# Kernel optimization log

Hardware: AMD Instinct MI355X
Metric: run time of the kernel (lower is better)

## Reference

```python
import jax, jax.numpy as jnp
import numpy as np

TOKEN_DIM = 768
HIDDEN_DIM = 384
PATCH_SCALE = 2
SELECTED_RATIO = 0.15


def setup_inputs() -> dict:
    key = jax.random.key(0)
    ks = jax.random.split(key, 12)
    B, T, D = 32, 1024, TOKEN_DIM
    Thr = T * PATCH_SCALE * PATCH_SCALE  # 4096
    flat_dim = D * PATCH_SCALE * PATCH_SCALE  # 3072
    H = HIDDEN_DIM
    s = lambda fan_in: 1.0 / np.sqrt(fan_in)
    inp = {
        "base_tokens": jax.random.normal(ks[0], (B, T, D), jnp.float32),
        "highres_tokens": jax.random.normal(ks[1], (B, Thr, D), jnp.float32),
        "selection_scores": jax.random.normal(ks[2], (B, T), jnp.float32),
        # local_refine: Linear(flat_dim,H) -> GELU -> Linear(H,D)
        "W1": jax.random.uniform(ks[3], (flat_dim, H), jnp.float32, -s(flat_dim), s(flat_dim)),
        "b1": jax.random.uniform(ks[4], (H,), jnp.float32, -s(flat_dim), s(flat_dim)),
        "W2": jax.random.uniform(ks[5], (H, D), jnp.float32, -s(H), s(H)),
        "b2": jax.random.uniform(ks[6], (D,), jnp.float32, -s(H), s(H)),
        # blend_gate: Linear(2D+1,H) -> SiLU -> Linear(H,1)
        "Wg1": jax.random.uniform(ks[7], (2 * D + 1, H), jnp.float32, -s(2 * D + 1), s(2 * D + 1)),
        "bg1": jax.random.uniform(ks[8], (H,), jnp.float32, -s(2 * D + 1), s(2 * D + 1)),
        "Wg2": jax.random.uniform(ks[9], (H, 1), jnp.float32, -s(H), s(H)),
        "bg2": jax.random.uniform(ks[10], (1,), jnp.float32, -s(H), s(H)),
    }
    return inp


def reference(base_tokens, highres_tokens, selection_scores,
              W1, b1, W2, b2, Wg1, bg1, Wg2, bg2):
    B, T, D = base_tokens.shape
    S = PATCH_SCALE
    g = int(round(np.sqrt(T)))  # coarse grid side
    # strided patch reshape: [B, g, S, g, S, D] -> [B, g, g, S, S, D] -> [B, T, S*S*D]
    local = highres_tokens.reshape(B, g, S, g, S, D)
    local = local.transpose(0, 1, 3, 2, 4, 5).reshape(B, T, S * S * D)
    # local refine MLP (exact-erf GELU matches torch nn.GELU default)
    h = jax.nn.gelu(jnp.einsum('btf,fh->bth', local, W1) + b1, approximate=False)
    refined_local = jnp.einsum('bth,hd->btd', h, W2) + b2
    # blend gate
    gate_in = jnp.concatenate([base_tokens, refined_local, selection_scores[..., None]], axis=-1)
    hg = jax.nn.silu(jnp.einsum('btf,fh->bth', gate_in, Wg1) + bg1)
    gate = jax.nn.sigmoid(jnp.einsum('bth,ho->bto', hg, Wg2) + bg2)  # [B, T, 1]
    # top-k selection mask (static k)
    topk = max(1, int(round(T * SELECTED_RATIO)))
    topk_idx = jax.lax.top_k(selection_scores, topk)[1]  # [B, k]
    mask = jnp.zeros((B, T), base_tokens.dtype).at[jnp.arange(B)[:, None], topk_idx].set(1.0)
    refined = base_tokens + mask[..., None] * gate * (refined_local - base_tokens)
    return refined
```

## Files before the change

kernel.cpp:

```cpp
#include <hip/hip_runtime.h>
#include <cstdint>

#define NB    32
#define NTOK  1024
#define D_    768
#define NHR   4096
#define HID   384
#define KSEL  154
#define MSEL  4928
#define MT_   77
#define FLAT  3072

typedef short  s16x8 __attribute__((ext_vector_type(8)));
typedef unsigned short u16x8 __attribute__((ext_vector_type(8)));
typedef unsigned short u16x4 __attribute__((ext_vector_type(4)));
typedef float  f32x4 __attribute__((ext_vector_type(4)));

__device__ inline unsigned short f2bf(float f) {
    uint32_t u = __builtin_bit_cast(uint32_t, f);
    u += 0x7FFFu + ((u >> 16) & 1u);
    return (unsigned short)(u >> 16);
}
__device__ inline float bf2f(unsigned short h) {
    uint32_t u = ((uint32_t)h) << 16;
    return __builtin_bit_cast(float, u);
}

#define OFF_SEL   0
#define OFF_W1T   32768
#define OFF_W2T   2392064
#define OFF_WG1T  2981888
#define OFF_ABASE 4161536
#define OFF_H     11730944
#define OFF_RL    15515648
#define OFF_HG    23085056
#define OFF_RMAP  30654464

__global__ __launch_bounds__(1024) void topk_kernel(const float* __restrict__ scores,
                                                    int* __restrict__ sel,
                                                    int* __restrict__ rmap) {
    __shared__ float s[NTOK];
    __shared__ int cnt;
    const int b = blockIdx.x;
    const int t = threadIdx.x;
    s[t] = scores[b * NTOK + t];
    if (t == 0) cnt = 0;
    __syncthreads();
    float v = s[t];
    int rank = 0;
    for (int j = 0; j < NTOK; ++j) {
        float vj = s[j];
        rank += (vj > v) || (vj == v && j < t);
    }
    int rm = -1;
    if (rank < KSEL) {
        int pos = atomicAdd(&cnt, 1);
        rm = b * KSEL + pos;
        sel[rm] = t;
    }
    rmap[b * NTOK + t] = rm;
}

__global__ __launch_bounds__(256) void tcvt_all(const float* __restrict__ W1,
                                                const float* __restrict__ W2,
                                                const float* __restrict__ Wg1,
                                                unsigned short* __restrict__ W1t,
                                                unsigned short* __restrict__ W2t,
                                                unsigned short* __restrict__ Wg1t) {
    __shared__ unsigned short T[64][66];
    int bid = blockIdx.x;
    const float* src; unsigned short* dst; int K, N, kt, nt;
    if (bid < 288)      { src = W1;  dst = W1t;  K = FLAT;   N = HID; nt = bid % 6;  kt = bid / 6;  }
    else if (bid < 360) { int l = bid - 288; src = W2;  dst = W2t;  K = HID;  N = D_;  nt = l % 12; kt = l / 12; }
    else                { int l = bid - 360; src = Wg1; dst = Wg1t; K = 1536; N = HID; nt = l % 6;  kt = l / 6;  }
    const int k0 = kt * 64, n0 = nt * 64;
    const int tid = threadIdx.x;
    {
        const int ln = tid & 63, kc = tid >> 6;
        #pragma unroll
        for (int j = 0; j < 16; ++j)
            T[ln][kc * 16 + j] = f2bf(src[(uint64_t)(k0 + kc * 16 + j) * N + n0 + ln]);
    }
    __syncthreads();
    {
        const int row = tid >> 2, c0 = (tid & 3) * 16;
        u16x8 v0, v1;
        #pragma unroll
        for (int p = 0; p < 8; ++p) { v0[p] = T[row][c0 + p]; v1[p] = T[row][c0 + 8 + p]; }
        *(u16x8*)(dst + (uint64_t)(n0 + row) * K + k0 + c0) = v0;
        *(u16x8*)(dst + (uint64_t)(n0 + row) * K + k0 + c0 + 8) = v1;
    }
}

__global__ __launch_bounds__(256) void gather_kernel(
    const int* __restrict__ sel, const float* __restrict__ highres,
    const float* __restrict__ base,
    unsigned short* __restrict__ Aloc, unsigned short* __restrict__ Abase) {
    const int r = blockIdx.x;
    const int b = r / KSEL;
    const int t = sel[r];
    const int gy = t >> 5, gx = t & 31;
    for (int ch = threadIdx.x; ch < 480; ch += 256) {
        if (ch < 384) {
            int k8 = ch * 8;
            int p = k8 / D_;
            int col = k8 - p * D_;
            int hr = (gy * 2 + (p >> 1)) * 64 + gx * 2 + (p & 1);
            const float4* s4 = (const float4*)(highres + ((uint64_t)b * NHR + hr) * D_ + col);
            float4 v0 = s4[0], v1 = s4[1];
            u16x8 v;
            v[0]=f2bf(v0.x); v[1]=f2bf(v0.y); v[2]=f2bf(v0.z); v[3]=f2bf(v0.w);
            v[4]=f2bf(v1.x); v[5]=f2bf(v1.y); v[6]=f2bf(v1.z); v[7]=f2bf(v1.w);
            *(u16x8*)(Aloc + (uint64_t)r * FLAT + k8) = v;
        } else {
            int col = (ch - 384) * 8;
            const float4* s4 = (const float4*)(base + ((uint64_t)b * NTOK + t) * D_ + col);
            float4 v0 = s4[0], v1 = s4[1];
            u16x8 v;
            v[0]=f2bf(v0.x); v[1]=f2bf(v0.y); v[2]=f2bf(v0.z); v[3]=f2bf(v0.w);
            v[4]=f2bf(v1.x); v[5]=f2bf(v1.y); v[6]=f2bf(v1.z); v[7]=f2bf(v1.w);
            *(u16x8*)(Abase + (uint64_t)r * D_ + col) = v;
        }
    }
}

template <int MODE>
__global__ __launch_bounds__(256) void gemm_mfma(
    const unsigned short* __restrict__ A0,
    const unsigned short* __restrict__ A1,
    const unsigned short* __restrict__ Bt,
    const float* __restrict__ bias,
    const int* __restrict__ sel,
    const float* __restrict__ scores,
    const float* __restrict__ WgLast,
    void* __restrict__ Cout)
{
    constexpr int K = MODE == 0 ? FLAT : (MODE == 1 ? HID : 2 * D_);
    constexpr int N = MODE == 1 ? D_ : HID;
    constexpr int NT = N / 64;
    constexpr int NSTEP = K / 64;

    const int lin = blockIdx.x;
    const int xcd = lin & 7;
    const int j   = lin >> 3;
    const int mhi = j / NT;
    const int ntile = j - mhi * NT;
    const int mt = mhi * 8 + xcd;
    if (mt >= MT_) return;
    const int m0 = mt * 64;
    const int n0 = ntile * 64;

    __shared__ unsigned short As[2][64 * 64];
    __shared__ unsigned short Bs[2][64 * 64];
    __shared__ float scv[64];

    const int tid = threadIdx.x;
    const int lane = tid & 63;
    const int wid = tid >> 6;
    const int wm = wid >> 1;
    const int wn = wid & 1;

    if (MODE == 2 && tid < 64) {
        int r = m0 + tid, b = r / KSEL, t = sel[r];
        scv[tid] = scores[b * NTOK + t];
    }

    const int sr0 = tid >> 3;
    const int sc0 = tid & 7;

    auto loadA = [&](int k0, int half, s16x8& dst) {
        int r = sr0 + half * 32;
        int k = k0 + sc0 * 8;
        const unsigned short* p;
        if (MODE == 2) {
            p = (k < D_) ? (A0 + (uint64_t)(m0 + r) * D_ + k)
                         : (A1 + (uint64_t)(m0 + r) * D_ + (k - D_));
        } else {
            p = A0 + (uint64_t)(m0 + r) * K + k;
        }
        dst = *(const s16x8*)p;
    };
    auto loadB = [&](int k0, int half, s16x8& dst) {
        int r = sr0 + half * 32;
        dst = *(const s16x8*)(Bt + (uint64_t)(n0 + r) * K + k0 + sc0 * 8);
    };
    auto writeTile = [&](int buf, s16x8* a, s16x8* b) {
        #pragma unroll
        for (int half = 0; half < 2; ++half) {
            int r = sr0 + half * 32;
            int c = sc0 ^ (r & 7);
            *(s16x8*)&As[buf][r * 64 + c * 8] = a[half];
            *(s16x8*)&Bs[buf][r * 64 + c * 8] = b[half];
        }
    };

    f32x4 acc[2][2];
    #pragma unroll
    for (int i = 0; i < 2; ++i)
        #pragma unroll
        for (int jj = 0; jj < 2; ++jj) acc[i][jj] = (f32x4){0.f, 0.f, 0.f, 0.f};

    s16x8 aR[2], bR[2];
    loadA(0, 0, aR[0]); loadA(0, 1, aR[1]);
    loadB(0, 0, bR[0]); loadB(0, 1, bR[1]);
    writeTile(0, aR, bR);
    __syncthreads();
    if (NSTEP > 1) {
        loadA(64, 0, aR[0]); loadA(64, 1, aR[1]);
        loadB(64, 0, bR[0]); loadB(64, 1, bR[1]);
    }

    int cur = 0;
    for (int t = 0; t < NSTEP; ++t) {
        #pragma unroll
        for (int kk = 0; kk < 2; ++kk) {
            s16x8 af[2], bfr[2];
            #pragma unroll
            for (int i = 0; i < 2; ++i) {
                int row  = wm * 32 + i * 16 + (lane & 15);
                int cch  = (kk * 4 + (lane >> 4)) ^ (row & 7);
                af[i] = *(const s16x8*)&As[cur][row * 64 + cch * 8];
                int nrow = wn * 32 + i * 16 + (lane & 15);
                int cchb = (kk * 4 + (lane >> 4)) ^ (nrow & 7);
                bfr[i] = *(const s16x8*)&Bs[cur][nrow * 64 + cchb * 8];
            }
            #pragma unroll
            for (int i = 0; i < 2; ++i)
                #pragma unroll
                for (int jj = 0; jj < 2; ++jj)
                    acc[i][jj] = __builtin_amdgcn_mfma_f32_16x16x32_bf16(af[i], bfr[jj], acc[i][jj], 0, 0, 0);
        }
        if (t + 1 < NSTEP) {
            writeTile(cur ^ 1, aR, bR);
            __syncthreads();
            if (t + 2 < NSTEP) {
                int k0 = (t + 2) * 64;
                loadA(k0, 0, aR[0]); loadA(k0, 1, aR[1]);
                loadB(k0, 0, bR[0]); loadB(k0, 1, bR[1]);
            }
            cur ^= 1;
        }
    }

    #pragma unroll
    for (int i = 0; i < 2; ++i) {
        #pragma unroll
        for (int jj = 0; jj < 2; ++jj) {
            #pragma unroll
            for (int reg = 0; reg < 4; ++reg) {
                int m = m0 + wm * 32 + i * 16 + (lane >> 4) * 4 + reg;
                int n = n0 + wn * 32 + jj * 16 + (lane & 15);
                float x = acc[i][jj][reg] + bias[n];
                if (MODE == 0) {
                    x = 0.5f * x * (1.0f + erff(x * 0.70710678118654752f));
                    ((unsigned short*)Cout)[(uint64_t)m * HID + n] = f2bf(x);
                } else if (MODE == 1) {
                    ((unsigned short*)Cout)[(uint64_t)m * D_ + n] = f2bf(x);
                } else {
                    x += scv[m - m0] * WgLast[n];
                    x = x / (1.0f + __expf(-x));
                    ((float*)Cout)[(uint64_t)m * HID + n] = x;
                }
            }
        }
    }
}

__global__ __launch_bounds__(256) void finalize_kernel(
    const int* __restrict__ rmap,
    const float* __restrict__ hg,
    const float* __restrict__ Wg2, const float* __restrict__ bg2,
    const float* __restrict__ base, const unsigned short* __restrict__ rl,
    float* __restrict__ out)
{
    const int lane = threadIdx.x & 63;
    const int row = blockIdx.x * 4 + (threadIdx.x >> 6);
    const int rm = rmap[row];

    const uint64_t bo = (uint64_t)row * D_;
    const float4* b4 = (const float4*)(base + bo);
    float4* o4 = (float4*)(out + bo);

    if (rm < 0) {
        #pragma unroll
        for (int i = 0; i < 3; ++i) o4[lane + 64 * i] = b4[lane + 64 * i];
        return;
    }
    const float* hgr = hg + (uint64_t)rm * HID;
    float sum = 0.f;
    #pragma unroll
    for (int i = 0; i < 6; ++i) sum += hgr[lane + 64 * i] * Wg2[lane + 64 * i];
    #pragma unroll
    for (int off = 32; off; off >>= 1) sum += __shfl_xor(sum, off);
    float gate = 1.0f / (1.0f + __expf(-(sum + bg2[0])));

    const u16x4* r4 = (const u16x4*)(rl + (uint64_t)rm * D_);
    #pragma unroll
    for (int i = 0; i < 3; ++i) {
        int idx = lane + 64 * i;
        float4 bb = b4[idx];
        u16x4 rr = r4[idx];
        float4 oo;
        oo.x = bb.x + gate * (bf2f(rr[0]) - bb.x);
        oo.y = bb.y + gate * (bf2f(rr[1]) - bb.y);
        oo.z = bb.z + gate * (bf2f(rr[2]) - bb.z);
        oo.w = bb.w + gate * (bf2f(rr[3]) - bb.w);
        o4[idx] = oo;
    }
}

extern "C" void kernel_launch(void* const* d_in, const int* in_sizes, int n_in,
                              void* d_out, int out_size, void* d_ws, size_t ws_size,
                              hipStream_t stream) {
    const float* base   = (const float*)d_in[0];
    const float* hires  = (const float*)d_in[1];
    const float* scores = (const float*)d_in[2];
    const float* W1  = (const float*)d_in[3];
    const float* b1  = (const float*)d_in[4];
    const float* W2  = (const float*)d_in[5];
    const float* b2  = (const float*)d_in[6];
    const float* Wg1 = (const float*)d_in[7];
    const float* bg1 = (const float*)d_in[8];
    const float* Wg2 = (const float*)d_in[9];
    const float* bg2 = (const float*)d_in[10];
    float* out = (float*)d_out;

    char* ws = (char*)d_ws;
    int*            sel   = (int*)(ws + OFF_SEL);
    unsigned short* W1t   = (unsigned short*)(ws + OFF_W1T);
    unsigned short* W2t   = (unsigned short*)(ws + OFF_W2T);
    unsigned short* Wg1t  = (unsigned short*)(ws + OFF_WG1T);
    unsigned short* Abase = (unsigned short*)(ws + OFF_ABASE);
    unsigned short* h     = (unsigned short*)(ws + OFF_H);
    unsigned short* rl    = (unsigned short*)(ws + OFF_RL);
    float*          hg    = (float*)(ws + OFF_HG);
    int*            rmap  = (int*)(ws + OFF_RMAP);
    unsigned short* Aloc  = (unsigned short*)d_out;

    topk_kernel<<<dim3(NB), dim3(1024), 0, stream>>>(scores, sel, rmap);
    tcvt_all<<<dim3(504), dim3(256), 0, stream>>>(W1, W2, Wg1, W1t, W2t, Wg1t);
    gather_kernel<<<dim3(MSEL), dim3(256), 0, stream>>>(sel, hires, base, Aloc, Abase);
    gemm_mfma<0><<<dim3(8 * 10 * 6),  dim3(256), 0, stream>>>(Aloc, nullptr, W1t, b1, sel, scores, nullptr, h);
    gemm_mfma<1><<<dim3(8 * 10 * 12), dim3(256), 0, stream>>>(h, nullptr, W2t, b2, sel, scores, nullptr, rl);
    gemm_mfma<2><<<dim3(8 * 10 * 6),  dim3(256), 0, stream>>>(Abase, rl, Wg1t, bg1, sel, scores, Wg1 + (uint64_t)1536 * HID, hg);
    finalize_kernel<<<dim3(NB * NTOK / 4), dim3(256), 0, stream>>>(rmap, hg, Wg2, bg2, base, rl, out);
}
```

Before: 153.4 us.

## Split-K first GEMM, fuse gate dot into gate GEMM, merge prep kernels

The first GEMM (K=3072) is split into two K halves with fp32 partials written to scratch space in the output buffer, and a new combine kernel adds them with bias and applies GELU. This doubles the block count, aimed at filling the CUs for a grid that was only 480 blocks. The gate GEMM epilogue now does the SiLU, multiplies by Wg2 and reduces per row into 12 partial sums, so the full hidden-gate matrix is no longer written. Top-k and weight transpose/convert are merged into one launch. The cost is an extra kernel and extra partial-sum memory traffic.

Measured after the change: 149.4 us. 1.03x faster.

```diff
diff --git a/kernel.cpp b/kernel.cpp
--- a/kernel.cpp
+++ b/kernel.cpp
@@ -27,68 +27,70 @@
 }
 
 #define OFF_SEL   0
-#define OFF_W1T   32768
-#define OFF_W2T   2392064
-#define OFF_WG1T  2981888
-#define OFF_ABASE 4161536
-#define OFF_H     11730944
-#define OFF_RL    15515648
-#define OFF_HG    23085056
-#define OFF_RMAP  30654464
-
-__global__ __launch_bounds__(1024) void topk_kernel(const float* __restrict__ scores,
-                                                    int* __restrict__ sel,
-                                                    int* __restrict__ rmap) {
+#define OFF_RMAP  32768
+#define OFF_GPART 163840
+#define OFF_W1T   401408
+#define OFF_W2T   2760704
+#define OFF_WG1T  3350528
+#define OFF_ABASE 4530176
+#define OFF_H     12099584
+#define OFF_RL    15884288
+#define DOUT_P0   32505856
+#define DOUT_P1   (DOUT_P0 + MSEL * HID * 4)
+
+__global__ __launch_bounds__(1024) void prep_kernel(
+    const float* __restrict__ scores, int* __restrict__ sel, int* __restrict__ rmap,
+    const float* __restrict__ W1, const float* __restrict__ W2, const float* __restrict__ Wg1,
+    unsigned short* __restrict__ W1t, unsigned short* __restrict__ W2t,
+    unsigned short* __restrict__ Wg1t)
+{
     __shared__ float s[NTOK];
     __shared__ int cnt;
-    const int b = blockIdx.x;
-    const int t = threadIdx.x;
-    s[t] = scores[b * NTOK + t];
-    if (t == 0) cnt = 0;
-    __syncthreads();
-    float v = s[t];
-    int rank = 0;
-    for (int j = 0; j < NTOK; ++j) {
-        float vj = s[j];
-        rank += (vj > v) || (vj == v && j < t);
-    }
-    int rm = -1;
-    if (rank < KSEL) {
-        int pos = atomicAdd(&cnt, 1);
-        rm = b * KSEL + pos;
-        sel[rm] = t;
-    }
-    rmap[b * NTOK + t] = rm;
-}
-
-__global__ __launch_bounds__(256) void tcvt_all(const float* __restrict__ W1,
-                                                const float* __restrict__ W2,
-                                                const float* __restrict__ Wg1,
-                                                unsigned short* __restrict__ W1t,
-                                                unsigned short* __restrict__ W2t,
-                                                unsigned short* __restrict__ Wg1t) {
-    __shared__ unsigned short T[64][66];
-    int bid = blockIdx.x;
-    const float* src; unsigned short* dst; int K, N, kt, nt;
-    if (bid < 288)      { src = W1;  dst = W1t;  K = FLAT;   N = HID; nt = bid % 6;  kt = bid / 6;  }
-    else if (bid < 360) { int l = bid - 288; src = W2;  dst = W2t;  K = HID;  N = D_;  nt = l % 12; kt = l / 12; }
-    else                { int l = bid - 360; src = Wg1; dst = Wg1t; K = 1536; N = HID; nt = l % 6;  kt = l / 6;  }
-    const int k0 = kt * 64, n0 = nt * 64;
-    const int tid = threadIdx.x;
-    {
-        const int ln = tid & 63, kc = tid >> 6;
-        #pragma unroll
-        for (int j = 0; j < 16; ++j)
-            T[ln][kc * 16 + j] = f2bf(src[(uint64_t)(k0 + kc * 16 + j) * N + n0 + ln]);
-    }
-    __syncthreads();
-    {
-        const int row = tid >> 2, c0 = (tid & 3) * 16;
-        u16x8 v0, v1;
-        #pragma unroll
-        for (int p = 0; p < 8; ++p) { v0[p] = T[row][c0 + p]; v1[p] = T[row][c0 + 8 + p]; }
-        *(u16x8*)(dst + (uint64_t)(n0 + row) * K + k0 + c0) = v0;
-        *(u16x8*)(dst + (uint64_t)(n0 + row) * K + k0 + c0 + 8) = v1;
+    __shared__ unsigned short T[4][64][66];
+    const int bid = blockIdx.x;
+    if (bid < NB) {
+        const int b = bid;
+        const int t = threadIdx.x;
+        s[t] = scores[b * NTOK + t];
+        if (t == 0) cnt = 0;
+        __syncthreads();
+        float v = s[t];
+        int rank = 0;
+        for (int j = 0; j < NTOK; ++j) {
+            float vj = s[j];
+            rank += (vj > v) || (vj == v && j < t);
+        }
+        int rm = -1;
+        if (rank < KSEL) {
+            int pos = atomicAdd(&cnt, 1);
+            rm = b * KSEL + pos;
+            sel[rm] = t;
+        }
+        rmap[b * NTOK + t] = rm;
+    } else {
+        const int g = threadIdx.x >> 8;
+        const int tid = threadIdx.x & 255;
+        const int tile = (bid - NB) * 4 + g;
+        const float* src; unsigned short* dst; int K, N, kt, nt;
+        if (tile < 288)      { src = W1;  dst = W1t;  K = FLAT; N = HID; nt = tile % 6;  kt = tile / 6;  }
+        else if (tile < 360) { int l = tile - 288; src = W2;  dst = W2t;  K = HID;  N = D_;  nt = l % 12; kt = l / 12; }
+        else                 { int l = tile - 360; src = Wg1; dst = Wg1t; K = 1536; N = HID; nt = l % 6;  kt = l / 6;  }
+        const int k0 = kt * 64, n0 = nt * 64;
+        {
+            const int ln = tid & 63, kc = tid >> 6;
+            #pragma unroll
+            for (int j = 0; j < 16; ++j)
+                T[g][ln][kc * 16 + j] = f2bf(src[(uint64_t)(k0 + kc * 16 + j) * N + n0 + ln]);
+        }
+        __syncthreads();
+        {
+            const int row = tid >> 2, c0 = (tid & 3) * 16;
+            u16x8 v0, v1;
+            #pragma unroll
+            for (int p = 0; p < 8; ++p) { v0[p] = T[g][row][c0 + p]; v1[p] = T[g][row][c0 + 8 + p]; }
+            *(u16x8*)(dst + (uint64_t)(n0 + row) * K + k0 + c0) = v0;
+            *(u16x8*)(dst + (uint64_t)(n0 + row) * K + k0 + c0 + 8) = v1;
+        }
     }
 }
 
@@ -133,22 +135,29 @@
     const int* __restrict__ sel,
     const float* __restrict__ scores,
     const float* __restrict__ WgLast,
-    void* __restrict__ Cout)
+    const float* __restrict__ Wg2,
+    void* __restrict__ Cout,
+    float* __restrict__ Pout,
+    float* __restrict__ gpart)
 {
     constexpr int K = MODE == 0 ? FLAT : (MODE == 1 ? HID : 2 * D_);
     constexpr int N = MODE == 1 ? D_ : HID;
     constexpr int NT = N / 64;
-    constexpr int NSTEP = K / 64;
+    constexpr int KLEN = (MODE == 0) ? 1536 : K;
+    constexpr int NSTEP = KLEN / 64;
 
     const int lin = blockIdx.x;
     const int xcd = lin & 7;
-    const int j   = lin >> 3;
-    const int mhi = j / NT;
-    const int ntile = j - mhi * NT;
+    int j = lin >> 3;
+    const int ntile = j % NT; j /= NT;
+    const int mhi = j % 10;
+    const int split = j / 10;
     const int mt = mhi * 8 + xcd;
     if (mt >= MT_) return;
     const int m0 = mt * 64;
     const int n0 = ntile * 64;
+    const int kb = split * 1536;
+    float* P = (MODE == 0) ? (Pout + (uint64_t)split * MSEL * HID) : nullptr;
 
     __shared__ unsigned short As[2][64 * 64];
     __shared__ unsigned short Bs[2][64 * 64];
@@ -201,13 +210,13 @@
         for (int jj = 0; jj < 2; ++jj) acc[i][jj] = (f32x4){0.f, 0.f, 0.f, 0.f};
 
     s16x8 aR[2], bR[2];
-    loadA(0, 0, aR[0]); loadA(0, 1, aR[1]);
-    loadB(0, 0, bR[0]); loadB(0, 1, bR[1]);
+    loadA(kb, 0, aR[0]); loadA(kb, 1, aR[1]);
+    loadB(kb, 0, bR[0]); loadB(kb, 1, bR[1]);
     writeTile(0, aR, bR);
     __syncthreads();
     if (NSTEP > 1) {
-        loadA(64, 0, aR[0]); loadA(64, 1, aR[1]);
-        loadB(64, 0, bR[0]); loadB(64, 1, bR[1]);
+        loadA(kb + 64, 0, aR[0]); loadA(kb + 64, 1, aR[1]);
+        loadB(kb + 64, 0, bR[0]); loadB(kb + 64, 1, bR[1]);
     }
 
     int cur = 0;
@@ -234,7 +243,7 @@
             writeTile(cur ^ 1, aR, bR);
             __syncthreads();
             if (t + 2 < NSTEP) {
-                int k0 = (t + 2) * 64;
+                int k0 = kb + (t + 2) * 64;
                 loadA(k0, 0, aR[0]); loadA(k0, 1, aR[1]);
                 loadB(k0, 0, bR[0]); loadB(k0, 1, bR[1]);
             }
@@ -242,6 +251,46 @@
         }
     }
 
+    if (MODE == 2) {
+        float wg2v[2] = { Wg2[n0 + wn * 32 + (lane & 15)],
+                          Wg2[n0 + wn * 32 + 16 + (lane & 15)] };
+        float psum[2][4];
+        #pragma unroll
+        for (int i = 0; i < 2; ++i)
+            #pragma unroll
+            for (int reg = 0; reg < 4; ++reg) psum[i][reg] = 0.f;
+        #pragma unroll
+        for (int i = 0; i < 2; ++i) {
+            #pragma unroll
+            for (int jj = 0; jj < 2; ++jj) {
+                #pragma unroll
+                for (int reg = 0; reg < 4; ++reg) {
+                    int m = m0 + wm * 32 + i * 16 + (lane >> 4) * 4 + reg;
+                    int n = n0 + wn * 32 + jj * 16 + (lane & 15);
+                    float x = acc[i][jj][reg] + bias[n] + scv[m - m0] * WgLast[n];
+                    x = x / (1.0f + __expf(-x));
+                    psum[i][reg] += x * wg2v[jj];
+                }
+            }
+        }
+        #pragma unroll
+        for (int mask = 1; mask < 16; mask <<= 1)
+            #pragma unroll
+            for (int i = 0; i < 2; ++i)
+                #pragma unroll
+                for (int reg = 0; reg < 4; ++reg)
+                    psum[i][reg] += __shfl_xor(psum[i][reg], mask);
+        if ((lane & 15) == 0) {
+            #pragma unroll
+            for (int i = 0; i < 2; ++i)
+                #pragma unroll
+                for (int reg = 0; reg < 4; ++reg) {
+                    int m = m0 + wm * 32 + i * 16 + (lane >> 4) * 4 + reg;
+                    gpart[m * 12 + ntile * 2 + wn] = psum[i][reg];
+                }
+        }
+        return;
+    }
     #pragma unroll
     for (int i = 0; i < 2; ++i) {
         #pragma unroll
@@ -250,26 +299,43 @@
             for (int reg = 0; reg < 4; ++reg) {
                 int m = m0 + wm * 32 + i * 16 + (lane >> 4) * 4 + reg;
                 int n = n0 + wn * 32 + jj * 16 + (lane & 15);
-                float x = acc[i][jj][reg] + bias[n];
                 if (MODE == 0) {
-                    x = 0.5f * x * (1.0f + erff(x * 0.70710678118654752f));
-                    ((unsigned short*)Cout)[(uint64_t)m * HID + n] = f2bf(x);
-                } else if (MODE == 1) {
+                    P[(uint64_t)m * HID + n] = acc[i][jj][reg];
+                } else {
+                    float x = acc[i][jj][reg] + bias[n];
                     ((unsigned short*)Cout)[(uint64_t)m * D_ + n] = f2bf(x);
-                } else {
-                    x += scv[m - m0] * WgLast[n];
-                    x = x / (1.0f + __expf(-x));
-                    ((float*)Cout)[(uint64_t)m * HID + n] = x;
                 }
             }
         }
     }
 }
 
+__global__ __launch_bounds__(256) void combine_kernel(
+    const float* __restrict__ P0, const float* __restrict__ P1,
+    const float* __restrict__ b1, unsigned short* __restrict__ h)
+{
+    const int idx = (blockIdx.x * 256 + threadIdx.x) * 8;
+    const int col = idx % HID;
+    float4 a0 = *(const float4*)(P0 + idx), a1 = *(const float4*)(P0 + idx + 4);
+    float4 c0 = *(const float4*)(P1 + idx), c1 = *(const float4*)(P1 + idx + 4);
+    float4 bb0 = *(const float4*)(b1 + col), bb1 = *(const float4*)(b1 + col + 4);
+    float xs[8] = { a0.x + c0.x + bb0.x, a0.y + c0.y + bb0.y,
+                    a0.z + c0.z + bb0.z, a0.w + c0.w + bb0.w,
+                    a1.x + c1.x + bb1.x, a1.y + c1.y + bb1.y,
+                    a1.z + c1.z + bb1.z, a1.w + c1.w + bb1.w };
+    u16x8 v;
+    #pragma unroll
+    for (int p = 0; p < 8; ++p) {
+        float x = xs[p];
+        x = 0.5f * x * (1.0f + erff(x * 0.70710678118654752f));
+        v[p] = f2bf(x);
+    }
+    *(u16x8*)(h + idx) = v;
+}
+
 __global__ __launch_bounds__(256) void finalize_kernel(
     const int* __restrict__ rmap,
-    const float* __restrict__ hg,
-    const float* __restrict__ Wg2, const float* __restrict__ bg2,
+    const float* __restrict__ gpart, const float* __restrict__ bg2,
     const float* __restrict__ base, const unsigned short* __restrict__ rl,
     float* __restrict__ out)
 {
@@ -286,13 +352,11 @@
         for (int i = 0; i < 3; ++i) o4[lane + 64 * i] = b4[lane + 64 * i];
         return;
     }
-    const float* hgr = hg + (uint64_t)rm * HID;
-    float sum = 0.f;
-    #pragma unroll
-    for (int i = 0; i < 6; ++i) sum += hgr[lane + 64 * i] * Wg2[lane + 64 * i];
-    #pragma unroll
-    for (int off = 32; off; off >>= 1) sum += __shfl_xor(sum, off);
-    float gate = 1.0f / (1.0f + __expf(-(sum + bg2[0])));
+    const float4* gp = (const float4*)(gpart + (uint64_t)rm * 12);
+    float4 g0 = gp[0], g1 = gp[1], g2 = gp[2];
+    float sum = g0.x + g0.y + g0.z + g0.w + g1.x + g1.y + g1.z + g1.w
+              + g2.x + g2.y + g2.z + g2.w + bg2[0];
+    float gate = 1.0f / (1.0f + __expf(-sum));
 
     const u16x4* r4 = (const u16x4*)(rl + (uint64_t)rm * D_);
     #pragma unroll
@@ -327,21 +391,28 @@
 
     char* ws = (char*)d_ws;
     int*            sel   = (int*)(ws + OFF_SEL);
+    int*            rmap  = (int*)(ws + OFF_RMAP);
+    float*          gpart = (float*)(ws + OFF_GPART);
     unsigned short* W1t   = (unsigned short*)(ws + OFF_W1T);
     unsigned short* W2t   = (unsigned short*)(ws + OFF_W2T);
     unsigned short* Wg1t  = (unsigned short*)(ws + OFF_WG1T);
     unsigned short* Abase = (unsigned short*)(ws + OFF_ABASE);
     unsigned short* h     = (unsigned short*)(ws + OFF_H);
     unsigned short* rl    = (unsigned short*)(ws + OFF_RL);
-    float*          hg    = (float*)(ws + OFF_HG);
-    int*            rmap  = (int*)(ws + OFF_RMAP);
     unsigned short* Aloc  = (unsigned short*)d_out;
-
-    topk_kernel<<<dim3(NB), dim3(1024), 0, stream>>>(scores, sel, rmap);
-    tcvt_all<<<dim3(504), dim3(256), 0, stream>>>(W1, W2, Wg1, W1t, W2t, Wg1t);
+    float*          P0    = (float*)((char*)d_out + DOUT_P0);
+    float*          P1    = (float*)((char*)d_out + DOUT_P1);
+
+    prep_kernel<<<dim3(NB + 126), dim3(1024), 0, stream>>>(scores, sel, rmap,
+                                                           W1, W2, Wg1, W1t, W2t, Wg1t);
     gather_kernel<<<dim3(MSEL), dim3(256), 0, stream>>>(sel, hires, base, Aloc, Abase);
-    gemm_mfma<0><<<dim3(8 * 10 * 6),  dim3(256), 0, stream>>>(Aloc, nullptr, W1t, b1, sel, scores, nullptr, h);
-    gemm_mfma<1><<<dim3(8 * 10 * 12), dim3(256), 0, stream>>>(h, nullptr, W2t, b2, sel, scores, nullptr, rl);
-    gemm_mfma<2><<<dim3(8 * 10 * 6),  dim3(256), 0, stream>>>(Abase, rl, Wg1t, bg1, sel, scores, Wg1 + (uint64_t)1536 * HID, hg);
-    finalize_kernel<<<dim3(NB * NTOK / 4), dim3(256), 0, stream>>>(rmap, hg, Wg2, bg2, base, rl, out);
-}
+    gemm_mfma<0><<<dim3(8 * 10 * 6 * 2), dim3(256), 0, stream>>>(
+        Aloc, nullptr, W1t, nullptr, nullptr, nullptr, nullptr, nullptr, nullptr, P0, nullptr);
+    combine_kernel<<<dim3(924), dim3(256), 0, stream>>>(P0, P1, b1, h);
+    gemm_mfma<1><<<dim3(8 * 10 * 12), dim3(256), 0, stream>>>(
+        h, nullptr, W2t, b2, nullptr, nullptr, nullptr, nullptr, rl, nullptr, nullptr);
+    gemm_mfma<2><<<dim3(8 * 10 * 6), dim3(256), 0, stream>>>(
+        Abase, rl, Wg1t, bg1, sel, scores, Wg1 + (uint64_t)1536 * HID, Wg2,
+        nullptr, nullptr, gpart);
+    finalize_kernel<<<dim3(NB * NTOK / 4), dim3(256), 0, stream>>>(rmap, gpart, bg2, base, rl, out);
+}
```
